# Performance work log

Hardware: AMD Instinct MI355X
Metric: run time of the kernel (lower is better)

## Reference

```python
import jax, jax.numpy as jnp
import numpy as np

K = 4096            # ca3_memory_slots
C = 2048            # ca3_code_dim
B = 8192            # query batch (episodes)
MAX_ITERS = 8       # cfg.pseudoinverse_iterations (spiking window T=8)
TOL = 1e-4          # cfg.convergence_tolerance
ALPHA_CLAMP = 5e-4  # torch.clamp(exp(log_scale), max=5e-4)


def setup_inputs() -> dict:
    key = jax.random.key(0)
    k1, k2, k3 = jax.random.split(key, 3)
    query = jax.random.normal(k1, (B, C), dtype=jnp.float32)
    # buffer init: torch.randn(K, C) * 0.01
    memory_mean = jax.random.normal(k2, (K, C), dtype=jnp.float32) * 0.01
    # nn.Parameter(torch.tensor(pseudoinverse_alpha_init)) -> scalar
    ben_israel_log_scale = jnp.float32(-0.5)
    return {"query": query, "memory_mean": memory_mean,
            "ben_israel_log_scale": ben_israel_log_scale}


def _ben_israel_pinv(A, log_scale):
    """Ben-Israel-Cohen iteration with masked early stopping (fixed trip count)."""
    A_fro_sq = jnp.sum(A * A)
    alpha = (1.0 / (A_fro_sq + 1e-8)) * jnp.minimum(jnp.exp(log_scale), ALPHA_CLAMP)
    pinv = alpha * A.T                       # (C, K)
    residual = jnp.array(jnp.inf, dtype=A.dtype)
    done = jnp.array(False)
    for _ in range(MAX_ITERS):
        pinv_new = 2.0 * pinv - pinv @ (A @ pinv)        # (C,K)
        recon = A @ (pinv_new @ A)                       # (K,C)
        res_new = jnp.linalg.norm(recon - A)             # Frobenius
        pinv = jnp.where(done, pinv, pinv_new)
        residual = jnp.where(done, residual, res_new)
        done = done | (res_new < TOL)
    return pinv, residual


def reference(query, memory_mean, ben_israel_log_scale):
    A = memory_mean                                      # (K, C)
    A_pinv, residual = _ben_israel_pinv(A, ben_israel_log_scale)  # (C, K)
    w = query @ A_pinv                                   # (B, K) addressing weights
    retrieved = w @ A                                    # (B, C) pattern completion
    return retrieved
```

## Files before the change

kernel.cpp:

```cpp
#include <hip/hip_runtime.h>
#include <hip/hip_bf16.h>
#include <cstdint>
#include <cstddef>


#define K_DIM 4096
#define C_DIM 2048
#define B_DIM 8192
#define SPLITK 4
#define KCHUNK (K_DIM / SPLITK)

typedef __bf16 bf16x8 __attribute__((ext_vector_type(8)));
typedef float f32x4 __attribute__((ext_vector_type(4)));

#define VMCNT(n) asm volatile("s_waitcnt vmcnt(" #n ")" ::: "memory")
#define LGKMCNT0 asm volatile("s_waitcnt lgkmcnt(0)" ::: "memory")
#define SBAR __builtin_amdgcn_s_barrier()

__device__ __forceinline__ void async_load16(const void* g, void* l) {
  __builtin_amdgcn_global_load_lds(
      (const __attribute__((address_space(1))) void*)g,
      (__attribute__((address_space(3))) void*)l, 16, 0, 0);
}

__global__ __launch_bounds__(256) void prep_kernel(
    const float* __restrict__ A, __hip_bfloat16* __restrict__ At,
    const float* __restrict__ q, __hip_bfloat16* __restrict__ qb,
    float* __restrict__ wsf) {
  const int b = blockIdx.x;
  const int t = threadIdx.x;
  if (b < 2048) {
    __shared__ __align__(16) __hip_bfloat16 Ts[64 * 68];
    const int c0 = (b & 31) * 64;
    const int k0 = (b >> 5) * 64;
    const int kk = t >> 4;
    const int c4 = (t & 15) * 4;
#pragma unroll
    for (int p = 0; p < 4; ++p) {
      const int k = kk + p * 16;
      const float4 v = *(const float4*)&A[(size_t)(k0 + k) * C_DIM + c0 + c4];
      Ts[(c4 + 0) * 68 + k] = __float2bfloat16(v.x);
      Ts[(c4 + 1) * 68 + k] = __float2bfloat16(v.y);
      Ts[(c4 + 2) * 68 + k] = __float2bfloat16(v.z);
      Ts[(c4 + 3) * 68 + k] = __float2bfloat16(v.w);
    }
    __syncthreads();
    const int c = t >> 2;
    const int seg = t & 3;
    const __hip_bfloat16* src = Ts + c * 68 + seg * 16;
    union { uint2 d[2]; uint4 qv; } o0, o1;
    o0.d[0] = *(const uint2*)(src + 0);
    o0.d[1] = *(const uint2*)(src + 4);
    o1.d[0] = *(const uint2*)(src + 8);
    o1.d[1] = *(const uint2*)(src + 12);
    __hip_bfloat16* dst = At + (size_t)(c0 + c) * K_DIM + k0 + seg * 16;
    *(uint4*)(dst + 0) = o0.qv;
    *(uint4*)(dst + 8) = o1.qv;
  } else {
    if (b == 2048 && t == 0) wsf[4] = 0.0f;
    const int n4 = B_DIM * C_DIM / 4;
    int tid = (b - 2048) * 256 + t;
    for (int i = tid; i < n4; i += 4096 * 256) {
      float4 v = ((const float4*)q)[i];
      __hip_bfloat16 o[4] = {__float2bfloat16(v.x), __float2bfloat16(v.y),
                             __float2bfloat16(v.z), __float2bfloat16(v.w)};
      *(uint2*)(qb + 4 * (size_t)i) = *(const uint2*)o;
    }
  }
}

__global__ __launch_bounds__(512, 2) void gemm_m3(
    const __hip_bfloat16* __restrict__ At, __hip_bfloat16* __restrict__ P) {
  constexpr int BK = 64;
  constexpr int NT = KCHUNK / BK;
  __shared__ __align__(16) __hip_bfloat16 As[2][256 * BK];
  __shared__ __align__(16) __hip_bfloat16 Bs[2][256 * BK];
  const int bid = blockIdx.x;
  const int sw = (bid & 7) * 32 + (bid >> 3);
  const int z = sw >> 6;
  const int rem = sw & 63;
  const int tm_i = rem >> 3;
  const int tn_i = rem & 7;
  const int tid = threadIdx.x;
  const int wave = tid >> 6, lane = tid & 63;
  const int tile_m = tm_i * 256, tile_n = tn_i * 256;
  const int kstart = z * KCHUNK;
  const int wm = (wave >> 2) * 128, wn = (wave & 3) * 64;
  const int lr = lane >> 3, lcl = (lane & 7) ^ lr;
  const __hip_bfloat16* aBase =
      At + (size_t)(tile_m + wave * 16 + lr) * K_DIM + kstart + lcl * 8;
  const __hip_bfloat16* bBase =
      At + (size_t)(tile_n + wave * 16 + lr) * K_DIM + kstart + lcl * 8;
  const int l15 = lane & 15, lg = lane >> 4, l7 = lane & 7;

  auto stA = [&](int buf, int h, int t) {
    const __hip_bfloat16* s = aBase + (size_t)(h * 128) * K_DIM + (size_t)t * BK;
    __hip_bfloat16* d = &As[buf][(h * 128 + wave * 16) * BK];
    async_load16(s, d);
    async_load16(s + (size_t)8 * K_DIM, d + 8 * BK);
  };
  auto stB = [&](int buf, int h, int t) {
    const __hip_bfloat16* s = bBase + (size_t)(h * 128) * K_DIM + (size_t)t * BK;
    __hip_bfloat16* d = &Bs[buf][(h * 128 + wave * 16) * BK];
    async_load16(s, d);
    async_load16(s + (size_t)8 * K_DIM, d + 8 * BK);
  };

  f32x4 acc[8][4] = {};

  stA(0, 0, 0); stA(0, 1, 0);
  stB(0, 0, 0); stB(0, 1, 0);
  stB(1, 0, 1); stB(1, 1, 1);
  VMCNT(4);
  SBAR;

  for (int t = 0; t < NT; ++t) {
    const int buf = t & 1;
    bf16x8 breg[4][2];
#pragma unroll
    for (int q = 0; q < 4; ++q) {
      bf16x8 af[2][2];
#pragma unroll
      for (int f = 0; f < 2; ++f)
#pragma unroll
        for (int s = 0; s < 2; ++s)
          af[f][s] = *(const bf16x8*)&As[buf][(wm + q * 32 + f * 16 + l15) * BK +
                                             ((((s << 2) | lg) ^ l7) << 3)];
      if (q == 0) {
#pragma unroll
        for (int j = 0; j < 4; ++j)
#pragma unroll
          for (int s = 0; s < 2; ++s)
            breg[j][s] = *(const bf16x8*)&Bs[buf][(wn + j * 16 + l15) * BK +
                                                 ((((s << 2) | lg) ^ l7) << 3)];
      }
      if (q == 0 && t + 1 < NT) stA(buf ^ 1, 0, t + 1);
      if (q == 1 && t + 1 < NT) stA(buf ^ 1, 1, t + 1);
      if (q == 2 && t + 2 < NT) stB(buf, 0, t + 2);
      if (q == 3) {
        if (t + 2 < NT) {
          stB(buf, 1, t + 2);
          VMCNT(4);
        } else {
          VMCNT(0);
        }
      }
      SBAR;
      LGKMCNT0;
      __builtin_amdgcn_s_setprio(1);
#pragma unroll
      for (int s = 0; s < 2; ++s)
#pragma unroll
        for (int f = 0; f < 2; ++f)
#pragma unroll
          for (int j = 0; j < 4; ++j)
            acc[q * 2 + f][j] = __builtin_amdgcn_mfma_f32_16x16x32_bf16(
                af[f][s], breg[j][s], acc[q * 2 + f][j], 0, 0, 0);
      __builtin_amdgcn_s_setprio(0);
      SBAR;
    }
  }

  __hip_bfloat16* Pz = P + (size_t)z * C_DIM * C_DIM;
#pragma unroll
  for (int m = 0; m < 8; ++m) {
    const int gm = tile_m + wm + m * 16 + lg * 4;
#pragma unroll
    for (int j = 0; j < 4; ++j) {
      const int gn = tile_n + wn + j * 16 + l15;
#pragma unroll
      for (int r = 0; r < 4; ++r)
        Pz[(size_t)(gm + r) * C_DIM + gn] = __float2bfloat16(acc[m][j][r]);
    }
  }
}

__global__ __launch_bounds__(256) void reduce4_kernel(
    const __hip_bfloat16* __restrict__ P, __hip_bfloat16* __restrict__ Mb,
    float* __restrict__ wsf) {
  const size_t CC = (size_t)C_DIM * C_DIM;
  const int n8 = (int)(CC / 8);
  int tid = blockIdx.x * blockDim.x + threadIdx.x;
  int stride = gridDim.x * blockDim.x;
  float tsum = 0.0f;
  bool hit = false;
  for (int i = tid; i < n8; i += stride) {
    float acc[8] = {};
#pragma unroll
    for (int z = 0; z < SPLITK; ++z) {
      uint4 raw = *(const uint4*)(P + z * CC + (size_t)i * 8);
      const __hip_bfloat16* h = (const __hip_bfloat16*)&raw;
#pragma unroll
      for (int j = 0; j < 8; ++j) acc[j] += __bfloat162float(h[j]);
    }
    __hip_bfloat16 o[8];
#pragma unroll
    for (int j = 0; j < 8; ++j) o[j] = __float2bfloat16(acc[j]);
    *(uint4*)(Mb + (size_t)i * 8) = *(const uint4*)o;
    const int e0 = 8 * i;
    const int g = e0 >> 11;
    const int d = g * (C_DIM + 1);
    if (d >= e0 && d < e0 + 8) {
      tsum += acc[d - e0];
      hit = true;
    }
  }
  if (hit) atomicAdd(wsf + 4, tsum);
}

__global__ __launch_bounds__(512, 2) void gemm_qm(
    const __hip_bfloat16* __restrict__ Ab, const __hip_bfloat16* __restrict__ Bb,
    float* __restrict__ Fp, const float* __restrict__ ls,
    const float* __restrict__ wsf) {
  constexpr int BK = 64;
  constexpr int NT = C_DIM / BK;
  __shared__ __align__(16) __hip_bfloat16 As[2][256 * BK];
  __shared__ __align__(16) __hip_bfloat16 Bs[2][256 * BK];
  const int bid = blockIdx.x;
  const int sw = (bid & 7) * 32 + (bid >> 3);
  const int tn_i = sw & 7;
  const int tm_i = sw >> 3;
  const int tid = threadIdx.x;
  const int wave = tid >> 6, lane = tid & 63;
  const int tile_m = tm_i * 256, tile_n = tn_i * 256;
  const int wm = (wave >> 2) * 128, wn = (wave & 3) * 64;
  const int lr = lane >> 3, lcl = (lane & 7) ^ lr;
  const __hip_bfloat16* aBase =
      Ab + (size_t)(tile_m + wave * 16 + lr) * C_DIM + lcl * 8;
  const __hip_bfloat16* bBase =
      Bb + (size_t)(tile_n + wave * 16 + lr) * C_DIM + lcl * 8;
  const int l15 = lane & 15, lg = lane >> 4, l7 = lane & 7;

  auto stA = [&](int buf, int h, int t) {
    const __hip_bfloat16* s = aBase + (size_t)(h * 128) * C_DIM + (size_t)t * BK;
    __hip_bfloat16* d = &As[buf][(h * 128 + wave * 16) * BK];
    async_load16(s, d);
    async_load16(s + (size_t)8 * C_DIM, d + 8 * BK);
  };
  auto stB = [&](int buf, int h, int t) {
    const __hip_bfloat16* s = bBase + (size_t)(h * 128) * C_DIM + (size_t)t * BK;
    __hip_bfloat16* d = &Bs[buf][(h * 128 + wave * 16) * BK];
    async_load16(s, d);
    async_load16(s + (size_t)8 * C_DIM, d + 8 * BK);
  };

  f32x4 acc[8][4] = {};
  bf16x8 af[4], bfr[4];

  auto rdA = [&](int buf, int mh, int s) {
#pragma unroll
    for (int f = 0; f < 4; ++f)
      af[f] = *(const bf16x8*)&As[buf][(wm + mh * 64 + f * 16 + l15) * BK +
                                       (((s * 4 + lg) ^ l7) * 8)];
  };
  auto rdB = [&](int buf, int s) {
#pragma unroll
    for (int j = 0; j < 4; ++j)
      bfr[j] = *(const bf16x8*)&Bs[buf][(wn + j * 16 + l15) * BK +
                                        (((s * 4 + lg) ^ l7) * 8)];
  };
  auto mm = [&](int mh) {
    __builtin_amdgcn_s_setprio(1);
#pragma unroll
    for (int f = 0; f < 4; ++f)
#pragma unroll
      for (int j = 0; j < 4; ++j)
        acc[mh * 4 + f][j] = __builtin_amdgcn_mfma_f32_16x16x32_bf16(
            af[f], bfr[j], acc[mh * 4 + f][j], 0, 0, 0);
    __builtin_amdgcn_s_setprio(0);
  };

  stA(0, 0, 0); stA(0, 1, 0);
  stB(0, 0, 0); stB(0, 1, 0);
  stB(1, 0, 1); stB(1, 1, 1);
  VMCNT(4);
  SBAR;

  for (int t = 0; t < NT; ++t) {
    const int buf = t & 1;
    rdA(buf, 0, 0);
    rdB(buf, 0);
    SBAR;
    if (t + 1 < NT) stA(buf ^ 1, 0, t + 1);
    LGKMCNT0;
    mm(0);
    rdA(buf, 1, 0);
    SBAR;
    if (t + 1 < NT) stA(buf ^ 1, 1, t + 1);
    LGKMCNT0;
    mm(1);
    rdA(buf, 0, 1);
    rdB(buf, 1);
    SBAR;
    LGKMCNT0;
    mm(0);
    rdA(buf, 1, 1);
    VMCNT(0);
    SBAR;
    if (t + 2 < NT) { stB(buf, 0, t + 2); stB(buf, 1, t + 2); }
    LGKMCNT0;
    mm(1);
  }

  const float c1 = 256.0f * fminf(expf(ls[0]), 5e-4f) / (wsf[4] + 1e-8f);
#pragma unroll
  for (int m = 0; m < 8; ++m) {
    const int gm = tile_m + wm + m * 16 + lg * 4;
#pragma unroll
    for (int j = 0; j < 4; ++j) {
      const int gn = tile_n + wn + j * 16 + l15;
#pragma unroll
      for (int r = 0; r < 4; ++r)
        Fp[(size_t)(gm + r) * C_DIM + gn] = c1 * acc[m][j][r];
    }
  }
}

extern "C" void kernel_launch(void* const* d_in, const int* in_sizes, int n_in,
                              void* d_out, int out_size, void* d_ws, size_t ws_size,
                              hipStream_t stream) {
  const float* query = (const float*)d_in[0];
  const float* A = (const float*)d_in[1];
  const float* ls = (const float*)d_in[2];
  float* out = (float*)d_out;

  char* ws = (char*)d_ws;
  float* wsf = (float*)ws;
  size_t off = 256;
  __hip_bfloat16* At = (__hip_bfloat16*)(ws + off);
  off += (size_t)C_DIM * K_DIM * 2;
  __hip_bfloat16* qb = (__hip_bfloat16*)(ws + off);
  off += (size_t)B_DIM * C_DIM * 2;
  __hip_bfloat16* Mb = (__hip_bfloat16*)(ws + off);

  __hip_bfloat16* P = (__hip_bfloat16*)out;

  prep_kernel<<<6144, 256, 0, stream>>>(A, At, query, qb, wsf);
  gemm_m3<<<256, 512, 0, stream>>>(At, P);
  reduce4_kernel<<<2048, 256, 0, stream>>>(P, Mb, wsf);
  gemm_qm<<<256, 512, 0, stream>>>(qb, Mb, out, ls, wsf);
}
```

Baseline: 276.4 us.

## Restructure gemm_qm main loop into 8-phase schedule with finer-grained LDS reads

Result: faster. 267.6 us (-3.2%).

```diff
diff --git a/kernel.cpp b/kernel.cpp
--- a/kernel.cpp
+++ b/kernel.cpp
@@ -214,6 +214,7 @@
     const float* __restrict__ wsf) {
   constexpr int BK = 64;
   constexpr int NT = C_DIM / BK;
+  constexpr int NIT = NT / 2;
   __shared__ __align__(16) __hip_bfloat16 As[2][256 * BK];
   __shared__ __align__(16) __hip_bfloat16 Bs[2][256 * BK];
   const int bid = blockIdx.x;
@@ -245,28 +246,34 @@
   };
 
   f32x4 acc[8][4] = {};
-  bf16x8 af[4], bfr[4];
-
-  auto rdA = [&](int buf, int mh, int s) {
-#pragma unroll
-    for (int f = 0; f < 4; ++f)
-      af[f] = *(const bf16x8*)&As[buf][(wm + mh * 64 + f * 16 + l15) * BK +
-                                       (((s * 4 + lg) ^ l7) * 8)];
-  };
-  auto rdB = [&](int buf, int s) {
+  bf16x8 breg[4][2], af[2][2];
+
+  auto rdA = [&](int buf, int q) {
+#pragma unroll
+    for (int f = 0; f < 2; ++f)
+#pragma unroll
+      for (int s = 0; s < 2; ++s)
+        af[f][s] = *(const bf16x8*)&As[buf][(wm + q * 32 + f * 16 + l15) * BK +
+                                           ((((s << 2) | lg) ^ l7) << 3)];
+  };
+  auto rdB = [&](int buf) {
 #pragma unroll
     for (int j = 0; j < 4; ++j)
-      bfr[j] = *(const bf16x8*)&Bs[buf][(wn + j * 16 + l15) * BK +
-                                        (((s * 4 + lg) ^ l7) * 8)];
-  };
-  auto mm = [&](int mh) {
+#pragma unroll
+      for (int s = 0; s < 2; ++s)
+        breg[j][s] = *(const bf16x8*)&Bs[buf][(wn + j * 16 + l15) * BK +
+                                             ((((s << 2) | lg) ^ l7) << 3)];
+  };
+  auto mm = [&](int q) {
     __builtin_amdgcn_s_setprio(1);
 #pragma unroll
-    for (int f = 0; f < 4; ++f)
-#pragma unroll
-      for (int j = 0; j < 4; ++j)
-        acc[mh * 4 + f][j] = __builtin_amdgcn_mfma_f32_16x16x32_bf16(
-            af[f], bfr[j], acc[mh * 4 + f][j], 0, 0, 0);
+    for (int s = 0; s < 2; ++s)
+#pragma unroll
+      for (int f = 0; f < 2; ++f)
+#pragma unroll
+        for (int j = 0; j < 4; ++j)
+          acc[q * 2 + f][j] = __builtin_amdgcn_mfma_f32_16x16x32_bf16(
+              af[f][s], breg[j][s], acc[q * 2 + f][j], 0, 0, 0);
     __builtin_amdgcn_s_setprio(0);
   };
 
@@ -276,30 +283,40 @@
   VMCNT(4);
   SBAR;
 
-  for (int t = 0; t < NT; ++t) {
-    const int buf = t & 1;
-    rdA(buf, 0, 0);
-    rdB(buf, 0);
-    SBAR;
-    if (t + 1 < NT) stA(buf ^ 1, 0, t + 1);
-    LGKMCNT0;
-    mm(0);
-    rdA(buf, 1, 0);
-    SBAR;
-    if (t + 1 < NT) stA(buf ^ 1, 1, t + 1);
-    LGKMCNT0;
-    mm(1);
-    rdA(buf, 0, 1);
-    rdB(buf, 1);
-    SBAR;
-    LGKMCNT0;
-    mm(0);
-    rdA(buf, 1, 1);
-    VMCNT(0);
-    SBAR;
-    if (t + 2 < NT) { stB(buf, 0, t + 2); stB(buf, 1, t + 2); }
-    LGKMCNT0;
-    mm(1);
+  for (int k = 0; k < NIT; ++k) {
+    const int t1 = 2 * k + 1;
+    const bool st2 = (2 * k + 2 < NT);
+    const bool st3 = (2 * k + 3 < NT);
+    rdA(0, 0); rdB(0);
+    stA(1, 0, t1);
+    VMCNT(6);
+    SBAR; LGKMCNT0; mm(0); SBAR;
+    rdA(0, 1);
+    stA(1, 1, t1);
+    SBAR; LGKMCNT0; mm(1); SBAR;
+    rdA(0, 2);
+    if (st2) stB(0, 0, 2 * k + 2);
+    SBAR; LGKMCNT0; mm(2); SBAR;
+    rdA(0, 3);
+    if (st2) stB(0, 1, 2 * k + 2);
+    SBAR; LGKMCNT0; mm(3); SBAR;
+    rdA(1, 0); rdB(1);
+    if (st2) {
+      stA(0, 0, 2 * k + 2);
+      VMCNT(6);
+    } else {
+      VMCNT(0);
+    }
+    SBAR; LGKMCNT0; mm(0); SBAR;
+    rdA(1, 1);
+    if (st2) stA(0, 1, 2 * k + 2);
+    SBAR; LGKMCNT0; mm(1); SBAR;
+    rdA(1, 2);
+    if (st3) stB(1, 0, 2 * k + 3);
+    SBAR; LGKMCNT0; mm(2); SBAR;
+    rdA(1, 3);
+    if (st3) stB(1, 1, 2 * k + 3);
+    SBAR; LGKMCNT0; mm(3); SBAR;
   }
 
   const float c1 = 256.0f * fminf(expf(ls[0]), 5e-4f) / (wsf[4] + 1e-8f);
```
